# Performance work log

Measured on AMD Instinct MI355X. Metric: run time of the kernel, lower is better.

The kernel has to match this reference:

```python
import jax, jax.numpy as jnp
import numpy as np

PD = 256            # pretrain_dim == dim_in (standard mode)
DZ = 128            # dim_z
PD2 = PD + 2        # feature dim after concatenating 2-d coords
FD = PD + 2 * PD2   # final_dim = 772
TEMP = float(DZ) ** 0.5
EPS = 1e-12
N1, N2 = 4096, 2048


def _lin_init(key, din, dout):
    w = jax.random.normal(key, (dout, din), jnp.float32) * 0.02
    b = jnp.zeros((dout,), jnp.float32)
    return w, b


def _lin(x, w, b):
    return x @ w.T + b


def setup_inputs() -> dict:
    key = jax.random.key(0)
    ks = jax.random.split(key, 13)
    lm_X = jax.random.normal(ks[0], (N1, PD), jnp.float32)
    lm_Y = jax.random.normal(ks[1], (N1, 2), jnp.float32)
    tg_X = jax.random.normal(ks[2], (N2, PD), jnp.float32)
    tg_Y = jax.random.normal(ks[3], (N2, 2), jnp.float32)
    lm_delay = jax.random.uniform(ks[4], (N1,), jnp.float32)
    tg_delay = jax.random.uniform(ks[5], (N2,), jnp.float32)
    aq_w, aq_b = _lin_init(ks[6], PD, DZ)    # att_attribute q proj
    ak_w, ak_b = _lin_init(ks[7], PD, DZ)    # att_attribute k proj
    w1_w, w1_b = _lin_init(ks[8], PD2, PD2)  # self.w_1
    w2_w, w2_b = _lin_init(ks[9], PD2, PD2)  # self.w_2
    pq_w, pq_b = _lin_init(ks[10], FD, DZ)   # pred attention q proj
    pk_w, pk_b = _lin_init(ks[11], PD, DZ)   # pred attention k proj
    pv_w, pv_b = _lin_init(ks[12], 2, 2)     # pred attention v proj
    gamma1 = jnp.ones((1, 1), jnp.float32)
    gamma2 = jnp.ones((1, 1), jnp.float32)
    gamma3 = jnp.ones((1, 1), jnp.float32)
    alpha = jnp.ones((1, 1), jnp.float32)
    beta = jnp.zeros((1, 1), jnp.float32)
    return dict(lm_X=lm_X, lm_Y=lm_Y, tg_X=tg_X, tg_Y=tg_Y,
                lm_delay=lm_delay, tg_delay=tg_delay,
                aq_w=aq_w, aq_b=aq_b, ak_w=ak_w, ak_b=ak_b,
                w1_w=w1_w, w1_b=w1_b, w2_w=w2_w, w2_b=w2_b,
                pq_w=pq_w, pq_b=pq_b, pk_w=pk_w, pk_b=pk_b,
                pv_w=pv_w, pv_b=pv_b,
                gamma1=gamma1, gamma2=gamma2, gamma3=gamma3,
                alpha=alpha, beta=beta)


def reference(lm_X, lm_Y, tg_X, tg_Y, lm_delay, tg_delay,
              aq_w, aq_b, ak_w, ak_b,
              w1_w, w1_b, w2_w, w2_b,
              pq_w, pq_b, pk_w, pk_b, pv_w, pv_b,
              gamma1, gamma2, gamma3, alpha, beta):
    n2 = tg_X.shape[0]
    a = alpha[0, 0]
    b0 = beta[0, 0]

    lm_feature = jnp.concatenate([lm_X, lm_Y], axis=1)            # [N1, PD2]
    tg_feature_0 = jnp.concatenate([tg_X, jnp.zeros((n2, 2), lm_X.dtype)], axis=1)
    router_0 = jnp.mean(lm_feature, axis=0)                        # [PD2]

    delay_score = jnp.exp(-gamma1[0, 0] * (a * lm_delay + b0))     # [N1]
    rou0 = jnp.exp(-gamma2[0, 0] * (a * tg_delay + b0))            # [N2]
    rou1 = jnp.exp(-gamma3[0, 0] * (a * tg_delay + b0))            # [N2]

    # SimpleAttention1: attribute score of targets over landmarks
    q = _lin(tg_X, aq_w, aq_b)
    k = _lin(lm_X, ak_w, ak_b)
    attr = jnp.exp(jax.nn.softmax((q / TEMP) @ k.T, axis=-1))      # [N2, N1]

    # Degree-normalized propagation of adj_matrix_0 (block-structured:
    # lm rows = identity, tg rows = [attr | I | rou0-col], router row = [delay | 0 | 1]).
    deg_tg0 = 1.0 + attr.sum(axis=1) + rou0                        # [N2]
    tg_prop0 = (attr @ lm_feature + tg_feature_0 + rou0[:, None] * router_0[None, :]) \
               / (deg_tg0 + EPS)[:, None]
    router_prop0 = (delay_score @ lm_feature + router_0) / (1.0 + delay_score.sum() + EPS)

    tg_feature_1 = _lin(tg_prop0, w1_w, w1_b)                      # [N2, PD2]
    router_1 = _lin(router_prop0[None, :], w1_w, w1_b)             # [1, PD2]

    # Second propagation: adj_matrix_1 = I + rou1 on tg->router column.
    tg_prop1 = (tg_feature_1 + rou1[:, None] * router_1) / (1.0 + rou1 + EPS)[:, None]
    tg_feature_2 = _lin(tg_prop1, w2_w, w2_b)                      # [N2, PD2]

    final_tg_feature = jnp.concatenate([tg_X, tg_feature_1, tg_feature_2], axis=-1)  # [N2, FD]

    # SimpleAttention2 (collaborative MLP prediction)
    q2 = _lin(final_tg_feature, pq_w, pq_b)
    k2 = _lin(lm_X, pk_w, pk_b)
    v2 = _lin(lm_Y, pv_w, pv_b)
    attn2 = jax.nn.softmax((q2 / TEMP) @ k2.T, axis=-1)            # [N2, N1]
    y_pred = attn2 @ v2                                            # [N2, 2]
    return y_pred, final_tg_feature
```

## Files before the change

### kernel.cpp

```cpp
#include <hip/hip_runtime.h>

#define N1 4096
#define N2 2048
#define PD 256
#define DZ 128
#define PD2 258
#define PD2P 264
#define FD 772
#define FDP 776
#define APN 272
#define APLD 72
#define SPLITS 16

typedef short s8v __attribute__((ext_vector_type(8)));
typedef float f32x4 __attribute__((ext_vector_type(4)));

__device__ __forceinline__ short f2b(float f) {
    union { float f; unsigned u; } v; v.f = f;
    unsigned r = v.u + 0x7fffu + ((v.u >> 16) & 1u);
    return (short)(r >> 16);
}
__device__ __forceinline__ float sb2f(short s) {
    union { unsigned u; float f; } v;
    v.u = ((unsigned)(unsigned short)s) << 16;
    return v.f;
}

constexpr int S0 = N1 * PD;
constexpr int S1 = S0 + N2 * PD;
constexpr int S2 = S1 + DZ * PD;
constexpr int S3 = S2 + 256 * 256;
constexpr int S4 = S3 + DZ * FDP;
constexpr int S5 = S4 + PD2 * PD2P;
constexpr int S6 = S5 + PD2 * PD2P;
constexpr int S7 = S6 + APN * N1;
constexpr int S8 = S7 + N1;
constexpr int S9 = S8 + 2048 + 8192 + 12288 + 256;

__global__ __launch_bounds__(256) void cvt_all(
    const float* __restrict__ lmX, const float* __restrict__ lmY,
    const float* __restrict__ tgX,
    const float* __restrict__ aqw, const float* __restrict__ akw,
    const float* __restrict__ pkw, const float* __restrict__ pqw,
    const float* __restrict__ w1w, const float* __restrict__ w2w,
    const float* __restrict__ lmd, const float* __restrict__ tgd,
    const float* __restrict__ g1, const float* __restrict__ g2,
    const float* __restrict__ g3, const float* __restrict__ al,
    const float* __restrict__ be,
    const float* __restrict__ pvw, const float* __restrict__ pvb,
    const float* __restrict__ akb, const float* __restrict__ pkb,
    short* __restrict__ lmXb, short* __restrict__ tgXb,
    short* __restrict__ aqwb, short* __restrict__ wkkb,
    short* __restrict__ pqwb,
    short* __restrict__ w1wb, short* __restrict__ w2wb,
    short* __restrict__ lmFTb,
    float* __restrict__ dscore, float* __restrict__ rou0,
    float* __restrict__ rou1, float* __restrict__ v2b,
    float* __restrict__ Z, short* __restrict__ finalFb,
    short* __restrict__ tgp1b, float* __restrict__ biasKK,
    float* __restrict__ outF)
{
    int i = blockIdx.x * 256 + threadIdx.x;
    if (i < S0) { lmXb[i] = f2b(lmX[i]); return; }
    if (i < S1) { int j = i - S0; int r = j >> 8, c = j & 255;
                  float v = tgX[j];
                  tgXb[j] = f2b(v);
                  outF[(size_t)r * FD + c] = v;
                  finalFb[(size_t)r * FDP + c] = f2b(v); return; }
    if (i < S2) { int j = i - S1; aqwb[j] = f2b(aqw[j]); return; }
    if (i < S3) { int j = i - S2; int r = j >> 8, c = j & 255;
                  wkkb[j] = f2b(r < 128 ? akw[r * 256 + c] : pkw[(r - 128) * 256 + c]);
                  return; }
    if (i < S4) { int j = i - S3; int r = j / FDP, c = j - r * FDP;
                  pqwb[j] = (c < FD) ? f2b(pqw[r * FD + c]) : (short)0; return; }
    if (i < S5) { int j = i - S4; int r = j / PD2P, c = j - r * PD2P;
                  w1wb[j] = (c < PD2) ? f2b(w1w[r * PD2 + c]) : (short)0; return; }
    if (i < S6) { int j = i - S5; int r = j / PD2P, c = j - r * PD2P;
                  w2wb[j] = (c < PD2) ? f2b(w2w[r * PD2 + c]) : (short)0; return; }
    if (i < S7) { int j = i - S6; int c = j >> 12, r = j & (N1 - 1);
                  float v = 0.f;
                  if (c < PD) v = lmX[r * PD + c];
                  else if (c < PD2) v = lmY[r * 2 + (c - PD)];
                  else if (c == PD2) v = 1.0f;
                  lmFTb[j] = f2b(v); return; }
    if (i < S8) { int j = i - S7;
                  float a = al[0], b = be[0];
                  dscore[j] = __expf(-g1[0] * (a * lmd[j] + b));
                  float y0 = lmY[2 * j], y1 = lmY[2 * j + 1];
                  v2b[2 * j]     = pvw[0] * y0 + pvw[1] * y1 + pvb[0];
                  v2b[2 * j + 1] = pvw[2] * y0 + pvw[3] * y1 + pvb[1];
                  if (j < N2) { float t = a * tgd[j] + b;
                                rou0[j] = __expf(-g2[0] * t);
                                rou1[j] = __expf(-g3[0] * t); }
                  return; }
    if (i < S9) { int j = i - S8;
                  if (j < 2048) { Z[j] = 0.f; return; }
                  j -= 2048;
                  if (j < 8192) { int r = j >> 2, c = FD + (j & 3);
                                  finalFb[(size_t)r * FDP + c] = 0; return; }
                  j -= 8192;
                  if (j < 12288) { int r = j / 6, c = PD2 + (j - r * 6);
                                   tgp1b[(size_t)r * PD2P + c] = 0; return; }
                  j -= 12288;
                  biasKK[j] = (j < 128) ? akb[j] : pkb[j - 128];
                  return; }
}

__global__ __launch_bounds__(256) void router_kernel(const short* __restrict__ lmFTb,
                                                     const float* __restrict__ dscore,
                                                     float* __restrict__ router0,
                                                     float* __restrict__ routerp0) {
    int c = blockIdx.x;
    const short* rowp = lmFTb + (size_t)c * N1;
    __shared__ float r1[256], r2[256], r3[256];
    int tid = threadIdx.x;
    float s1 = 0.f, s2 = 0.f, s3 = 0.f;
    for (int i = tid; i < N1; i += 256) {
        float v = sb2f(rowp[i]);
        float d = dscore[i];
        s1 += v; s2 += d * v; s3 += d;
    }
    r1[tid] = s1; r2[tid] = s2; r3[tid] = s3; __syncthreads();
    for (int o = 128; o > 0; o >>= 1) {
        if (tid < o) { r1[tid] += r1[tid + o]; r2[tid] += r2[tid + o]; r3[tid] += r3[tid + o]; }
        __syncthreads();
    }
    if (tid == 0) {
        float r0 = r1[0] / (float)N1;
        router0[c] = r0;
        routerp0[c] = (r2[0] + r0) / (1.f + r3[0] + 1e-12f);
    }
}

__global__ __launch_bounds__(256) void router1_kernel(const float* __restrict__ rp0,
                                                      const float* __restrict__ w1w,
                                                      const float* __restrict__ w1b,
                                                      float* __restrict__ router1) {
    for (int c = threadIdx.x; c < PD2; c += 256) {
        float s = w1b[c];
        const float* wr = w1w + (size_t)c * PD2;
        for (int k = 0; k < PD2; ++k) s += rp0[k] * wr[k];
        router1[c] = s;
    }
}

__global__ __launch_bounds__(256) void proj_gemm(
    const short* __restrict__ A, const short* __restrict__ B,
    const float* __restrict__ bias, short* __restrict__ outB,
    int M, int N, int KP, int ldo, float scale)
{
    __shared__ short Als[64][40];
    __shared__ short Bls[64][40];
    const int tid = threadIdx.x;
    const int wave = tid >> 6, lane = tid & 63;
    const int wm = wave >> 1, wn = wave & 1;
    const int lm = lane & 15, lq = lane >> 4;
    const int row0 = blockIdx.y * 64, col0 = blockIdx.x * 64;
    f32x4 acc[2][2];
    const f32x4 zero4 = {0.f, 0.f, 0.f, 0.f};
#pragma unroll
    for (int mt = 0; mt < 2; ++mt)
#pragma unroll
        for (int nt = 0; nt < 2; ++nt) acc[mt][nt] = zero4;
    const s8v zero8 = {0, 0, 0, 0, 0, 0, 0, 0};
    for (int k0 = 0; k0 < KP; k0 += 32) {
        {
            int r = tid >> 2, cg = tid & 3;
            int gk = k0 + cg * 8;
            s8v va = zero8, vb = zero8;
            if (row0 + r < M && gk < KP) va = *(const s8v*)(A + (size_t)(row0 + r) * KP + gk);
            if (col0 + r < N && gk < KP) vb = *(const s8v*)(B + (size_t)(col0 + r) * KP + gk);
            *(s8v*)(&Als[r][cg * 8]) = va;
            *(s8v*)(&Bls[r][cg * 8]) = vb;
        }
        __syncthreads();
        s8v af[2], bf[2];
#pragma unroll
        for (int mt = 0; mt < 2; ++mt)
            af[mt] = *(const s8v*)(&Als[wm * 32 + mt * 16 + lm][lq * 8]);
#pragma unroll
        for (int nt = 0; nt < 2; ++nt)
            bf[nt] = *(const s8v*)(&Bls[wn * 32 + nt * 16 + lm][lq * 8]);
#pragma unroll
        for (int mt = 0; mt < 2; ++mt)
#pragma unroll
            for (int nt = 0; nt < 2; ++nt)
                acc[mt][nt] = __builtin_amdgcn_mfma_f32_16x16x32_bf16(
                    af[mt], bf[nt], acc[mt][nt], 0, 0, 0);
        __syncthreads();
    }
#pragma unroll
    for (int mt = 0; mt < 2; ++mt)
#pragma unroll
        for (int nt = 0; nt < 2; ++nt) {
            int c = col0 + wn * 32 + nt * 16 + lm;
            if (c >= N) continue;
            float bv = bias ? bias[c] : 0.f;
#pragma unroll
            for (int i = 0; i < 4; ++i) {
                int r = row0 + wm * 32 + mt * 16 + lq * 4 + i;
                if (r >= M) continue;
                outB[(size_t)r * ldo + c] = f2b(scale * (acc[mt][nt][i] + bv));
            }
        }
}

__global__ __launch_bounds__(256) void scores_e(
    const short* __restrict__ Q,
    const short* __restrict__ Kk,
    short* __restrict__ E, float* __restrict__ Z)
{
    __shared__ short Als[128][40];
    __shared__ short Bls[128][40];
    const int tid = threadIdx.x;
    const int wave = tid >> 6, lane = tid & 63;
    const int wm = wave >> 1, wn = wave & 1;
    const int lm = lane & 15, lq = lane >> 4;
    const int row0 = blockIdx.y * 128, col0 = blockIdx.x * 128;
    f32x4 acc[4][4];
    const f32x4 zero4 = {0.f, 0.f, 0.f, 0.f};
#pragma unroll
    for (int mt = 0; mt < 4; ++mt)
#pragma unroll
        for (int nt = 0; nt < 4; ++nt) acc[mt][nt] = zero4;
    for (int k0 = 0; k0 < 128; k0 += 32) {
#pragma unroll
        for (int l = 0; l < 2; ++l) {
            int id = l * 256 + tid;
            int r = id >> 2, cg = id & 3;
            int gk = k0 + cg * 8;
            *(s8v*)(&Als[r][cg * 8]) = *(const s8v*)(Q + (size_t)(row0 + r) * DZ + gk);
            *(s8v*)(&Bls[r][cg * 8]) = *(const s8v*)(Kk + (size_t)(col0 + r) * 256 + gk);
        }
        __syncthreads();
        s8v af[4], bf[4];
#pragma unroll
        for (int mt = 0; mt < 4; ++mt)
            af[mt] = *(const s8v*)(&Als[wm * 64 + mt * 16 + lm][lq * 8]);
#pragma unroll
        for (int nt = 0; nt < 4; ++nt)
            bf[nt] = *(const s8v*)(&Bls[wn * 64 + nt * 16 + lm][lq * 8]);
#pragma unroll
        for (int mt = 0; mt < 4; ++mt)
#pragma unroll
            for (int nt = 0; nt < 4; ++nt)
                acc[mt][nt] = __builtin_amdgcn_mfma_f32_16x16x32_bf16(
                    af[mt], bf[nt], acc[mt][nt], 0, 0, 0);
        __syncthreads();
    }
#pragma unroll
    for (int mt = 0; mt < 4; ++mt)
#pragma unroll
        for (int i = 0; i < 4; ++i) {
            int r = row0 + wm * 64 + mt * 16 + lq * 4 + i;
            float rs = 0.f;
#pragma unroll
            for (int nt = 0; nt < 4; ++nt) {
                int c = col0 + wn * 64 + nt * 16 + lm;
                float e = __expf(acc[mt][nt][i]);
                E[(size_t)r * N1 + c] = f2b(e);
                rs += e;
            }
#pragma unroll
            for (int msk = 1; msk < 16; msk <<= 1) rs += __shfl_xor(rs, msk, 64);
            if (lm == 0) atomicAdd(&Z[r], rs);
        }
}

__global__ __launch_bounds__(256) void ap_gemm(const short* __restrict__ E,
                                               const float* __restrict__ Z,
                                               const short* __restrict__ lmFTb,
                                               float* __restrict__ part)
{
    __shared__ short Als[128 * APLD];
    __shared__ short Bls[APN * APLD];
    const int tid = threadIdx.x;
    const int wave = tid >> 6, lane = tid & 63;
    const int lm = lane & 15, lq = lane >> 4;
    const int s = blockIdx.x;
    const int row0 = blockIdx.y * 128;
    const int kbase = s * (N1 / SPLITS);
    f32x4 acc0[17], acc1[17];
    const f32x4 zero4 = {0.f, 0.f, 0.f, 0.f};
#pragma unroll
    for (int nt = 0; nt < 17; ++nt) { acc0[nt] = zero4; acc1[nt] = zero4; }

    for (int it = 0; it < (N1 / SPLITS) / 64; ++it) {
        int k0 = kbase + it * 64;
#pragma unroll
        for (int l = 0; l < 4; ++l) {
            int id = l * 256 + tid;
            int r = id >> 3, g = id & 7;
            s8v ev = *(const s8v*)(E + (size_t)(row0 + r) * N1 + k0 + g * 8);
            float invZ = __builtin_amdgcn_rcpf(Z[row0 + r]);
            s8v av;
#pragma unroll
            for (int j = 0; j < 8; ++j)
                av[j] = f2b(__expf(sb2f(ev[j]) * invZ));
            *(s8v*)(&Als[r * APLD + g * 8]) = av;
        }
#pragma unroll
        for (int l = 0; l < 9; ++l) {
            int id = l * 256 + tid;
            if (id < APN * 8) {
                int r = id >> 3, g = id & 7;
                *(s8v*)(&Bls[r * APLD + g * 8]) =
                    *(const s8v*)(lmFTb + (size_t)r * N1 + k0 + g * 8);
            }
        }
        __syncthreads();
        s8v a00 = *(const s8v*)(&Als[(wave * 32 + lm) * APLD + lq * 8]);
        s8v a01 = *(const s8v*)(&Als[(wave * 32 + lm) * APLD + 32 + lq * 8]);
        s8v a10 = *(const s8v*)(&Als[(wave * 32 + 16 + lm) * APLD + lq * 8]);
        s8v a11 = *(const s8v*)(&Als[(wave * 32 + 16 + lm) * APLD + 32 + lq * 8]);
#pragma unroll
        for (int nt = 0; nt < 17; ++nt) {
            s8v b0 = *(const s8v*)(&Bls[(nt * 16 + lm) * APLD + lq * 8]);
            s8v b1 = *(const s8v*)(&Bls[(nt * 16 + lm) * APLD + 32 + lq * 8]);
            acc0[nt] = __builtin_amdgcn_mfma_f32_16x16x32_bf16(a00, b0, acc0[nt], 0, 0, 0);
            acc0[nt] = __builtin_amdgcn_mfma_f32_16x16x32_bf16(a01, b1, acc0[nt], 0, 0, 0);
            acc1[nt] = __builtin_amdgcn_mfma_f32_16x16x32_bf16(a10, b0, acc1[nt], 0, 0, 0);
            acc1[nt] = __builtin_amdgcn_mfma_f32_16x16x32_bf16(a11, b1, acc1[nt], 0, 0, 0);
        }
        __syncthreads();
    }
    float* op = part + (size_t)s * N2 * APN;
#pragma unroll
    for (int nt = 0; nt < 17; ++nt) {
        int c = nt * 16 + lm;
#pragma unroll
        for (int i = 0; i < 4; ++i) {
            int r = row0 + wave * 32 + lq * 4 + i;
            op[(size_t)r * APN + c] = acc0[nt][i];
            op[(size_t)(r + 16) * APN + c] = acc1[nt][i];
        }
    }
}

__global__ __launch_bounds__(256) void fix_tgp0(const float* __restrict__ part,
                                                const float* __restrict__ tgX,
                                                const float* __restrict__ rou0,
                                                const float* __restrict__ router0,
                                                short* __restrict__ outb) {
    int r = blockIdx.x;
    int tid = threadIdx.x;
    __shared__ float sAsum;
    float s0 = 0.f, s1 = 0.f;
#pragma unroll
    for (int s = 0; s < SPLITS; ++s)
        s0 += part[((size_t)s * N2 + r) * APN + tid];
    if (tid < 8) {
#pragma unroll
        for (int s = 0; s < SPLITS; ++s)
            s1 += part[((size_t)s * N2 + r) * APN + 256 + tid];
    }
    if (tid == 2) sAsum = s1;
    __syncthreads();
    float ro = rou0[r];
    float inv = 1.f / (1.f + sAsum + ro + 1e-12f);
    {
        float v = (s0 + tgX[(size_t)r * PD + tid] + ro * router0[tid]) * inv;
        outb[(size_t)r * PD2P + tid] = f2b(v);
    }
    if (tid < 8) {
        int c = 256 + tid;
        float v = 0.f;
        if (c < PD2) v = (s1 + ro * router0[c]) * inv;
        outb[(size_t)r * PD2P + c] = f2b(v);
    }
}

__global__ __launch_bounds__(256) void w_gemm(
    const short* __restrict__ A, const short* __restrict__ B,
    const float* __restrict__ bias,
    float* __restrict__ outFcol, short* __restrict__ fFbcol,
    const float* __restrict__ rou1, const float* __restrict__ router1,
    short* __restrict__ tgp1b)
{
    __shared__ short Als[64][40];
    __shared__ short Bls[64][40];
    const int tid = threadIdx.x;
    const int wave = tid >> 6, lane = tid & 63;
    const int wm = wave >> 1, wn = wave & 1;
    const int lm = lane & 15, lq = lane >> 4;
    const int row0 = blockIdx.y * 64, col0 = blockIdx.x * 64;
    f32x4 acc[2][2];
    const f32x4 zero4 = {0.f, 0.f, 0.f, 0.f};
#pragma unroll
    for (int mt = 0; mt < 2; ++mt)
#pragma unroll
        for (int nt = 0; nt < 2; ++nt) acc[mt][nt] = zero4;
    const s8v zero8 = {0, 0, 0, 0, 0, 0, 0, 0};
    for (int k0 = 0; k0 < PD2P; k0 += 32) {
        {
            int r = tid >> 2, cg = tid & 3;
            int gk = k0 + cg * 8;
            s8v va = zero8, vb = zero8;
            if (gk < PD2P) {
                va = *(const s8v*)(A + (size_t)(row0 + r) * PD2P + gk);
                if (col0 + r < PD2) vb = *(const s8v*)(B + (size_t)(col0 + r) * PD2P + gk);
            }
            *(s8v*)(&Als[r][cg * 8]) = va;
            *(s8v*)(&Bls[r][cg * 8]) = vb;
        }
        __syncthreads();
        s8v af[2], bf[2];
#pragma unroll
        for (int mt = 0; mt < 2; ++mt)
            af[mt] = *(const s8v*)(&Als[wm * 32 + mt * 16 + lm][lq * 8]);
#pragma unroll
        for (int nt = 0; nt < 2; ++nt)
            bf[nt] = *(const s8v*)(&Bls[wn * 32 + nt * 16 + lm][lq * 8]);
#pragma unroll
        for (int mt = 0; mt < 2; ++mt)
#pragma unroll
            for (int nt = 0; nt < 2; ++nt)
                acc[mt][nt] = __builtin_amdgcn_mfma_f32_16x16x32_bf16(
                    af[mt], bf[nt], acc[mt][nt], 0, 0, 0);
        __syncthreads();
    }
#pragma unroll
    for (int mt = 0; mt < 2; ++mt)
#pragma unroll
        for (int nt = 0; nt < 2; ++nt) {
            int c = col0 + wn * 32 + nt * 16 + lm;
            if (c >= PD2) continue;
            float bv = bias[c];
            float rc = router1 ? router1[c] : 0.f;
#pragma unroll
            for (int i = 0; i < 4; ++i) {
                int r = row0 + wm * 32 + mt * 16 + lq * 4 + i;
                float v = acc[mt][nt][i] + bv;
                outFcol[(size_t)r * FD + c] = v;
                fFbcol[(size_t)r * FDP + c] = f2b(v);
                if (tgp1b) {
                    float ro = rou1[r];
                    float t = (v + ro * rc) / (1.f + ro + 1e-12f);
                    tgp1b[(size_t)r * PD2P + c] = f2b(t);
                }
            }
        }
}

__global__ __launch_bounds__(256) void attn2_flash(
    const short* __restrict__ Q,
    const short* __restrict__ Kk,
    const float* __restrict__ V, float* __restrict__ part2)
{
    __shared__ short Qls[64 * 136];
    __shared__ short Kls[64 * 136];
    __shared__ float Vls[128];
    const int tid = threadIdx.x;
    const int wave = tid >> 6, lane = tid & 63;
    const int lm = lane & 15, lq = lane >> 4;
    const int chunk = blockIdx.x;
    const int row0 = blockIdx.y * 64;
#pragma unroll
    for (int l = 0; l < 4; ++l) {
        int id = l * 256 + tid;
        int r = id >> 4, g = id & 15;
        *(s8v*)(&Qls[r * 136 + g * 8]) = *(const s8v*)(Q + (size_t)(row0 + r) * DZ + g * 8);
    }
    __syncthreads();
    s8v af[4];
#pragma unroll
    for (int ks = 0; ks < 4; ++ks)
        af[ks] = *(const s8v*)(&Qls[(wave * 16 + lm) * 136 + ks * 32 + lq * 8]);
    float z[4] = {0.f, 0.f, 0.f, 0.f}, y0[4] = {0.f, 0.f, 0.f, 0.f}, y1[4] = {0.f, 0.f, 0.f, 0.f};

    for (int t = 0; t < 8; ++t) {
        int col0 = chunk * 512 + t * 64;
        __syncthreads();
#pragma unroll
        for (int l = 0; l < 4; ++l) {
            int id = l * 256 + tid;
            int r = id >> 4, g = id & 15;
            *(s8v*)(&Kls[r * 136 + g * 8]) =
                *(const s8v*)(Kk + (size_t)(col0 + r) * 256 + 128 + g * 8);
        }
        if (tid < 128) Vls[tid] = V[col0 * 2 + tid];
        __syncthreads();
        f32x4 acc[4];
        const f32x4 zero4 = {0.f, 0.f, 0.f, 0.f};
#pragma unroll
        for (int nt = 0; nt < 4; ++nt) acc[nt] = zero4;
#pragma unroll
        for (int nt = 0; nt < 4; ++nt)
#pragma unroll
            for (int ks = 0; ks < 4; ++ks) {
                s8v bf = *(const s8v*)(&Kls[(nt * 16 + lm) * 136 + ks * 32 + lq * 8]);
                acc[nt] = __builtin_amdgcn_mfma_f32_16x16x32_bf16(af[ks], bf, acc[nt], 0, 0, 0);
            }
        float v0[4], v1[4];
#pragma unroll
        for (int nt = 0; nt < 4; ++nt) {
            v0[nt] = Vls[(nt * 16 + lm) * 2];
            v1[nt] = Vls[(nt * 16 + lm) * 2 + 1];
        }
#pragma unroll
        for (int i = 0; i < 4; ++i) {
            float e0 = __expf(acc[0][i]), e1 = __expf(acc[1][i]);
            float e2 = __expf(acc[2][i]), e3 = __expf(acc[3][i]);
            float pz = e0 + e1 + e2 + e3;
            float py0 = e0 * v0[0] + e1 * v0[1] + e2 * v0[2] + e3 * v0[3];
            float py1 = e0 * v1[0] + e1 * v1[1] + e2 * v1[2] + e3 * v1[3];
#pragma unroll
            for (int msk = 1; msk < 16; msk <<= 1) {
                pz  += __shfl_xor(pz, msk, 64);
                py0 += __shfl_xor(py0, msk, 64);
                py1 += __shfl_xor(py1, msk, 64);
            }
            z[i] += pz; y0[i] += py0; y1[i] += py1;
        }
    }
    if (lm == 0) {
#pragma unroll
        for (int i = 0; i < 4; ++i) {
            int r = row0 + wave * 16 + lq * 4 + i;
            float* p = part2 + ((size_t)r * 8 + chunk) * 4;
            p[0] = z[i]; p[1] = y0[i]; p[2] = y1[i];
        }
    }
}

__global__ void attn2_combine(const float* __restrict__ part2, float* __restrict__ out) {
    int r = blockIdx.x * blockDim.x + threadIdx.x;
    if (r >= N2) return;
    const float* p = part2 + (size_t)r * 32;
    float Zt = 0.f, Y0 = 0.f, Y1 = 0.f;
#pragma unroll
    for (int c = 0; c < 8; ++c) {
        Zt += p[c * 4]; Y0 += p[c * 4 + 1]; Y1 += p[c * 4 + 2];
    }
    out[2 * r] = Y0 / Zt;
    out[2 * r + 1] = Y1 / Zt;
}

extern "C" void kernel_launch(void* const* d_in, const int* in_sizes, int n_in,
                              void* d_out, int out_size, void* d_ws, size_t ws_size,
                              hipStream_t stream) {
    const float* lm_X = (const float*)d_in[0];
    const float* lm_Y = (const float*)d_in[1];
    const float* tg_X = (const float*)d_in[2];
    const float* lm_delay = (const float*)d_in[4];
    const float* tg_delay = (const float*)d_in[5];
    const float* aq_w = (const float*)d_in[6];
    const float* aq_b = (const float*)d_in[7];
    const float* ak_w = (const float*)d_in[8];
    const float* ak_b = (const float*)d_in[9];
    const float* w1_w = (const float*)d_in[10];
    const float* w1_b = (const float*)d_in[11];
    const float* w2_w = (const float*)d_in[12];
    const float* w2_b = (const float*)d_in[13];
    const float* pq_w = (const float*)d_in[14];
    const float* pq_b = (const float*)d_in[15];
    const float* pk_w = (const float*)d_in[16];
    const float* pk_b = (const float*)d_in[17];
    const float* pv_w = (const float*)d_in[18];
    const float* pv_b = (const float*)d_in[19];
    const float* g1 = (const float*)d_in[20];
    const float* g2 = (const float*)d_in[21];
    const float* g3 = (const float*)d_in[22];
    const float* al = (const float*)d_in[23];
    const float* be = (const float*)d_in[24];

    float* out = (float*)d_out;
    float* outF = out + (size_t)N2 * 2;

    char* base = (char*)d_ws;
    size_t off = 0;
    auto allocF = [&](size_t n) -> float* {
        float* p = (float*)(base + off);
        off += (n * 4 + 255) / 256 * 256;
        return p;
    };
    auto allocS = [&](size_t n) -> short* {
        short* p = (short*)(base + off);
        off += (n * 2 + 255) / 256 * 256;
        return p;
    };

    short* E        = allocS((size_t)N2 * N1);
    float* appart   = allocF((size_t)SPLITS * N2 * APN);
    short* lmFTb    = allocS((size_t)APN * N1);
    short* lmXb     = allocS((size_t)N1 * PD);
    short* tgXb     = allocS((size_t)N2 * PD);
    short* qb_b     = allocS((size_t)N2 * DZ);
    short* kk       = allocS((size_t)N1 * 256);
    short* q2_b     = allocS((size_t)N2 * DZ);
    short* tgp0b    = allocS((size_t)N2 * PD2P);
    short* tgp1b    = allocS((size_t)N2 * PD2P);
    short* finalFb  = allocS((size_t)N2 * FDP);
    short* aqwb     = allocS((size_t)DZ * PD);
    short* wkkb     = allocS((size_t)256 * 256);
    short* pqwb     = allocS((size_t)DZ * FDP);
    short* w1wb     = allocS((size_t)PD2 * PD2P);
    short* w2wb     = allocS((size_t)PD2 * PD2P);
    float* v2b      = allocF((size_t)N1 * 2);
    float* part2    = allocF((size_t)N2 * 32);
    float* Zbuf     = allocF(N2);
    float* biasKK   = allocF(256);
    float* router0  = allocF(PD2);
    float* routerp0 = allocF(PD2);
    float* router1  = allocF(PD2);
    float* dscore   = allocF(N1);
    float* rou0     = allocF(N2);
    float* rou1     = allocF(N2);

    const float INV_TEMP = 0.08838834764831845f;

    hipLaunchKernelGGL(cvt_all, dim3((S9 + 255) / 256), dim3(256), 0, stream,
                       lm_X, lm_Y, tg_X, aq_w, ak_w, pk_w, pq_w, w1_w, w2_w,
                       lm_delay, tg_delay, g1, g2, g3, al, be, pv_w, pv_b, ak_b, pk_b,
                       lmXb, tgXb, aqwb, wkkb, pqwb, w1wb, w2wb, lmFTb,
                       dscore, rou0, rou1, v2b, Zbuf, finalFb, tgp1b, biasKK, outF);
    hipLaunchKernelGGL(router_kernel, dim3(PD2), dim3(256), 0, stream,
                       lmFTb, dscore, router0, routerp0);
    hipLaunchKernelGGL(router1_kernel, dim3(1), dim3(256), 0, stream,
                       routerp0, w1_w, w1_b, router1);

    hipLaunchKernelGGL(proj_gemm, dim3(4, 64), dim3(256), 0, stream,
                       lmXb, wkkb, biasKK, kk, N1, 256, PD, 256, 1.f);
    hipLaunchKernelGGL(proj_gemm, dim3(2, 32), dim3(256), 0, stream,
                       tgXb, aqwb, aq_b, qb_b, N2, DZ, PD, DZ, INV_TEMP);
    hipLaunchKernelGGL(scores_e, dim3(32, 16), dim3(256), 0, stream, qb_b, kk, E, Zbuf);
    hipLaunchKernelGGL(ap_gemm, dim3(SPLITS, N2 / 128), dim3(256), 0, stream,
                       E, Zbuf, lmFTb, appart);
    hipLaunchKernelGGL(fix_tgp0, dim3(N2), dim3(256), 0, stream,
                       appart, tg_X, rou0, router0, tgp0b);
    hipLaunchKernelGGL(w_gemm, dim3(5, 32), dim3(256), 0, stream,
                       tgp0b, w1wb, w1_b, outF + 256, finalFb + 256, rou1, router1, tgp1b);
    hipLaunchKernelGGL(w_gemm, dim3(5, 32), dim3(256), 0, stream,
                       tgp1b, w2wb, w2_b, outF + 514, finalFb + 514,
                       nullptr, nullptr, nullptr);
    hipLaunchKernelGGL(proj_gemm, dim3(2, 32), dim3(256), 0, stream,
                       finalFb, pqwb, pq_b, q2_b, N2, DZ, FDP, DZ, INV_TEMP);
    hipLaunchKernelGGL(attn2_flash, dim3(8, N2 / 64), dim3(256), 0, stream,
                       q2_b, kk, v2b, part2);
    hipLaunchKernelGGL(attn2_combine, dim3((N2 + 255) / 256), dim3(256), 0, stream,
                       part2, out);
}
```

Measured before the change: 252.2 us.

## Fuse router, projection and combine kernels; convert weights inline; bf16 partials

Merges the router reductions with the K/Q projection GEMMs into one kernel that converts fp32 inputs to bf16 while staging into LDS. This drops the separate bf16 copies of lmX, tgX and the projection weights. It also folds router1 into the scores kernel as an extra block, makes the ap_gemm partials bf16 with a new 512-thread launch, and replaces attn2_combine with a last-block-done atomic reduction. The goal is fewer launches and less intermediate memory traffic, at the cost of precision in the partials and an extra memset.

```diff
diff --git a/kernel.cpp b/kernel.cpp
--- a/kernel.cpp
+++ b/kernel.cpp
@@ -26,64 +26,51 @@
     return v.f;
 }
 
-constexpr int S0 = N1 * PD;
-constexpr int S1 = S0 + N2 * PD;
-constexpr int S2 = S1 + DZ * PD;
-constexpr int S3 = S2 + 256 * 256;
-constexpr int S4 = S3 + DZ * FDP;
-constexpr int S5 = S4 + PD2 * PD2P;
-constexpr int S6 = S5 + PD2 * PD2P;
-constexpr int S7 = S6 + APN * N1;
-constexpr int S8 = S7 + N1;
-constexpr int S9 = S8 + 2048 + 8192 + 12288 + 256;
+constexpr int R0 = N2 * PD;
+constexpr int R1 = R0 + PD2 * PD2P;
+constexpr int R2 = R1 + PD2 * PD2P;
+constexpr int R3 = R2 + DZ * FDP;
+constexpr int R4 = R3 + APN * N1;
+constexpr int R5 = R4 + 4096;
+constexpr int R6 = R5 + 2048;
+constexpr int R7 = R6 + N2 * 4;
+constexpr int R8 = R7 + N2 * 6;
 
 __global__ __launch_bounds__(256) void cvt_all(
     const float* __restrict__ lmX, const float* __restrict__ lmY,
     const float* __restrict__ tgX,
-    const float* __restrict__ aqw, const float* __restrict__ akw,
-    const float* __restrict__ pkw, const float* __restrict__ pqw,
-    const float* __restrict__ w1w, const float* __restrict__ w2w,
+    const float* __restrict__ pqw, const float* __restrict__ w1w,
+    const float* __restrict__ w2w,
     const float* __restrict__ lmd, const float* __restrict__ tgd,
     const float* __restrict__ g1, const float* __restrict__ g2,
     const float* __restrict__ g3, const float* __restrict__ al,
     const float* __restrict__ be,
     const float* __restrict__ pvw, const float* __restrict__ pvb,
-    const float* __restrict__ akb, const float* __restrict__ pkb,
-    short* __restrict__ lmXb, short* __restrict__ tgXb,
-    short* __restrict__ aqwb, short* __restrict__ wkkb,
-    short* __restrict__ pqwb,
     short* __restrict__ w1wb, short* __restrict__ w2wb,
-    short* __restrict__ lmFTb,
+    short* __restrict__ pqwb, short* __restrict__ lmFTb,
     float* __restrict__ dscore, float* __restrict__ rou0,
     float* __restrict__ rou1, float* __restrict__ v2b,
     float* __restrict__ Z, short* __restrict__ finalFb,
-    short* __restrict__ tgp1b, float* __restrict__ biasKK,
-    float* __restrict__ outF)
+    short* __restrict__ tgp1b, float* __restrict__ outF)
 {
     int i = blockIdx.x * 256 + threadIdx.x;
-    if (i < S0) { lmXb[i] = f2b(lmX[i]); return; }
-    if (i < S1) { int j = i - S0; int r = j >> 8, c = j & 255;
-                  float v = tgX[j];
-                  tgXb[j] = f2b(v);
+    if (i < R0) { int r = i >> 8, c = i & 255;
+                  float v = tgX[i];
                   outF[(size_t)r * FD + c] = v;
                   finalFb[(size_t)r * FDP + c] = f2b(v); return; }
-    if (i < S2) { int j = i - S1; aqwb[j] = f2b(aqw[j]); return; }
-    if (i < S3) { int j = i - S2; int r = j >> 8, c = j & 255;
-                  wkkb[j] = f2b(r < 128 ? akw[r * 256 + c] : pkw[(r - 128) * 256 + c]);
-                  return; }
-    if (i < S4) { int j = i - S3; int r = j / FDP, c = j - r * FDP;
+    if (i < R1) { int j = i - R0; int r = j / PD2P, c = j - r * PD2P;
+                  w1wb[j] = (c < PD2) ? f2b(w1w[r * PD2 + c]) : (short)0; return; }
+    if (i < R2) { int j = i - R1; int r = j / PD2P, c = j - r * PD2P;
+                  w2wb[j] = (c < PD2) ? f2b(w2w[r * PD2 + c]) : (short)0; return; }
+    if (i < R3) { int j = i - R2; int r = j / FDP, c = j - r * FDP;
                   pqwb[j] = (c < FD) ? f2b(pqw[r * FD + c]) : (short)0; return; }
-    if (i < S5) { int j = i - S4; int r = j / PD2P, c = j - r * PD2P;
-                  w1wb[j] = (c < PD2) ? f2b(w1w[r * PD2 + c]) : (short)0; return; }
-    if (i < S6) { int j = i - S5; int r = j / PD2P, c = j - r * PD2P;
-                  w2wb[j] = (c < PD2) ? f2b(w2w[r * PD2 + c]) : (short)0; return; }
-    if (i < S7) { int j = i - S6; int c = j >> 12, r = j & (N1 - 1);
+    if (i < R4) { int j = i - R3; int c = j >> 12, r = j & (N1 - 1);
                   float v = 0.f;
-                  if (c < PD) v = lmX[r * PD + c];
+                  if (c < PD) v = lmX[(size_t)r * PD + c];
                   else if (c < PD2) v = lmY[r * 2 + (c - PD)];
                   else if (c == PD2) v = 1.0f;
                   lmFTb[j] = f2b(v); return; }
-    if (i < S8) { int j = i - S7;
+    if (i < R5) { int j = i - R4;
                   float a = al[0], b = be[0];
                   dscore[j] = __expf(-g1[0] * (a * lmd[j] + b));
                   float y0 = lmY[2 * j], y1 = lmY[2 * j + 1];
@@ -93,132 +80,167 @@
                                 rou0[j] = __expf(-g2[0] * t);
                                 rou1[j] = __expf(-g3[0] * t); }
                   return; }
-    if (i < S9) { int j = i - S8;
-                  if (j < 2048) { Z[j] = 0.f; return; }
-                  j -= 2048;
-                  if (j < 8192) { int r = j >> 2, c = FD + (j & 3);
-                                  finalFb[(size_t)r * FDP + c] = 0; return; }
-                  j -= 8192;
-                  if (j < 12288) { int r = j / 6, c = PD2 + (j - r * 6);
-                                   tgp1b[(size_t)r * PD2P + c] = 0; return; }
-                  j -= 12288;
-                  biasKK[j] = (j < 128) ? akb[j] : pkb[j - 128];
-                  return; }
-}
-
-__global__ __launch_bounds__(256) void router_kernel(const short* __restrict__ lmFTb,
-                                                     const float* __restrict__ dscore,
-                                                     float* __restrict__ router0,
-                                                     float* __restrict__ routerp0) {
-    int c = blockIdx.x;
-    const short* rowp = lmFTb + (size_t)c * N1;
-    __shared__ float r1[256], r2[256], r3[256];
-    int tid = threadIdx.x;
-    float s1 = 0.f, s2 = 0.f, s3 = 0.f;
-    for (int i = tid; i < N1; i += 256) {
-        float v = sb2f(rowp[i]);
-        float d = dscore[i];
-        s1 += v; s2 += d * v; s3 += d;
-    }
-    r1[tid] = s1; r2[tid] = s2; r3[tid] = s3; __syncthreads();
-    for (int o = 128; o > 0; o >>= 1) {
-        if (tid < o) { r1[tid] += r1[tid + o]; r2[tid] += r2[tid + o]; r3[tid] += r3[tid + o]; }
-        __syncthreads();
-    }
-    if (tid == 0) {
-        float r0 = r1[0] / (float)N1;
-        router0[c] = r0;
-        routerp0[c] = (r2[0] + r0) / (1.f + r3[0] + 1e-12f);
-    }
-}
-
-__global__ __launch_bounds__(256) void router1_kernel(const float* __restrict__ rp0,
-                                                      const float* __restrict__ w1w,
-                                                      const float* __restrict__ w1b,
-                                                      float* __restrict__ router1) {
-    for (int c = threadIdx.x; c < PD2; c += 256) {
-        float s = w1b[c];
-        const float* wr = w1w + (size_t)c * PD2;
-        for (int k = 0; k < PD2; ++k) s += rp0[k] * wr[k];
-        router1[c] = s;
-    }
-}
-
-__global__ __launch_bounds__(256) void proj_gemm(
-    const short* __restrict__ A, const short* __restrict__ B,
-    const float* __restrict__ bias, short* __restrict__ outB,
-    int M, int N, int KP, int ldo, float scale)
+    if (i < R6) { Z[i - R5] = 0.f; return; }
+    if (i < R7) { int j = i - R6; int r = j >> 2;
+                  finalFb[(size_t)r * FDP + FD + (j & 3)] = 0; return; }
+    if (i < R8) { int j = i - R7; int r = j / 6;
+                  tgp1b[(size_t)r * PD2P + PD2 + (j - r * 6)] = 0; return; }
+}
+
+__global__ __launch_bounds__(256) void rkq_kernel(
+    const float* __restrict__ lmX, const float* __restrict__ tgX,
+    const float* __restrict__ aqw, const float* __restrict__ aqb,
+    const float* __restrict__ akw, const float* __restrict__ akb,
+    const float* __restrict__ pkw, const float* __restrict__ pkb,
+    const short* __restrict__ lmFTb, const float* __restrict__ dscore,
+    float* __restrict__ router0, float* __restrict__ routerp0,
+    short* __restrict__ kk, short* __restrict__ qb)
 {
-    __shared__ short Als[64][40];
-    __shared__ short Bls[64][40];
-    const int tid = threadIdx.x;
-    const int wave = tid >> 6, lane = tid & 63;
-    const int wm = wave >> 1, wn = wave & 1;
+    __shared__ __align__(16) short LDS[5120];
+    const int j = blockIdx.x, tid = threadIdx.x;
+    const int lane = tid & 63, wv = tid >> 6;
+    const int wm = wv >> 1, wn = wv & 1;
     const int lm = lane & 15, lq = lane >> 4;
-    const int row0 = blockIdx.y * 64, col0 = blockIdx.x * 64;
-    f32x4 acc[2][2];
     const f32x4 zero4 = {0.f, 0.f, 0.f, 0.f};
-#pragma unroll
-    for (int mt = 0; mt < 2; ++mt)
-#pragma unroll
-        for (int nt = 0; nt < 2; ++nt) acc[mt][nt] = zero4;
-    const s8v zero8 = {0, 0, 0, 0, 0, 0, 0, 0};
-    for (int k0 = 0; k0 < KP; k0 += 32) {
-        {
-            int r = tid >> 2, cg = tid & 3;
-            int gk = k0 + cg * 8;
-            s8v va = zero8, vb = zero8;
-            if (row0 + r < M && gk < KP) va = *(const s8v*)(A + (size_t)(row0 + r) * KP + gk);
-            if (col0 + r < N && gk < KP) vb = *(const s8v*)(B + (size_t)(col0 + r) * KP + gk);
-            *(s8v*)(&Als[r][cg * 8]) = va;
-            *(s8v*)(&Bls[r][cg * 8]) = vb;
-        }
-        __syncthreads();
-        s8v af[2], bf[2];
+
+    if (j < 258) {
+        float* r1 = (float*)LDS;
+        float* r2 = r1 + 256;
+        float* r3 = r2 + 256;
+        const short* rowp = lmFTb + (size_t)j * N1;
+        float s1 = 0.f, s2 = 0.f, s3 = 0.f;
+        for (int i = tid; i < N1; i += 256) {
+            float v = sb2f(rowp[i]);
+            float d = dscore[i];
+            s1 += v; s2 += d * v; s3 += d;
+        }
+        r1[tid] = s1; r2[tid] = s2; r3[tid] = s3; __syncthreads();
+        for (int o = 128; o > 0; o >>= 1) {
+            if (tid < o) { r1[tid] += r1[tid + o]; r2[tid] += r2[tid + o]; r3[tid] += r3[tid + o]; }
+            __syncthreads();
+        }
+        if (tid == 0) {
+            float r0v = r1[0] / (float)N1;
+            router0[j] = r0v;
+            routerp0[j] = (r2[0] + r0v) / (1.f + r3[0] + 1e-12f);
+        }
+        return;
+    }
+    short* Als = LDS;
+    short* Bls = LDS + 64 * 40;
+    f32x4 acc[2][2] = {{zero4, zero4}, {zero4, zero4}};
+    const int r = tid >> 2, cgp = tid & 3;
+    if (j < 514) {
+        int jt = j - 258;
+        int row0 = (jt >> 2) * 64, col0 = (jt & 3) * 64;
+        for (int k0 = 0; k0 < 256; k0 += 32) {
+            int gk = k0 + cgp * 8;
+            const float* ap = lmX + (size_t)(row0 + r) * PD + gk;
+            int c = col0 + r;
+            const float* bp = (c < 128) ? akw + (size_t)c * PD + gk
+                                        : pkw + (size_t)(c - 128) * PD + gk;
+            s8v va, vb;
+#pragma unroll
+            for (int q = 0; q < 8; ++q) { va[q] = f2b(ap[q]); vb[q] = f2b(bp[q]); }
+            *(s8v*)(Als + r * 40 + cgp * 8) = va;
+            *(s8v*)(Bls + r * 40 + cgp * 8) = vb;
+            __syncthreads();
+            s8v af[2], bf[2];
+#pragma unroll
+            for (int mt = 0; mt < 2; ++mt)
+                af[mt] = *(const s8v*)(Als + (wm * 32 + mt * 16 + lm) * 40 + lq * 8);
+#pragma unroll
+            for (int nt = 0; nt < 2; ++nt)
+                bf[nt] = *(const s8v*)(Bls + (wn * 32 + nt * 16 + lm) * 40 + lq * 8);
+#pragma unroll
+            for (int mt = 0; mt < 2; ++mt)
+#pragma unroll
+                for (int nt = 0; nt < 2; ++nt)
+                    acc[mt][nt] = __builtin_amdgcn_mfma_f32_16x16x32_bf16(
+                        af[mt], bf[nt], acc[mt][nt], 0, 0, 0);
+            __syncthreads();
+        }
 #pragma unroll
         for (int mt = 0; mt < 2; ++mt)
-            af[mt] = *(const s8v*)(&Als[wm * 32 + mt * 16 + lm][lq * 8]);
-#pragma unroll
-        for (int nt = 0; nt < 2; ++nt)
-            bf[nt] = *(const s8v*)(&Bls[wn * 32 + nt * 16 + lm][lq * 8]);
+#pragma unroll
+            for (int nt = 0; nt < 2; ++nt) {
+                int c = col0 + wn * 32 + nt * 16 + lm;
+                float bv = (c < 128) ? akb[c] : pkb[c - 128];
+#pragma unroll
+                for (int i = 0; i < 4; ++i) {
+                    int rr = row0 + wm * 32 + mt * 16 + lq * 4 + i;
+                    kk[(size_t)rr * 256 + c] = f2b(acc[mt][nt][i] + bv);
+                }
+            }
+    } else {
+        int jt = j - 514;
+        int row0 = (jt >> 1) * 64, col0 = (jt & 1) * 64;
+        for (int k0 = 0; k0 < 256; k0 += 32) {
+            int gk = k0 + cgp * 8;
+            const float* ap = tgX + (size_t)(row0 + r) * PD + gk;
+            const float* bp = aqw + (size_t)(col0 + r) * PD + gk;
+            s8v va, vb;
+#pragma unroll
+            for (int q = 0; q < 8; ++q) { va[q] = f2b(ap[q]); vb[q] = f2b(bp[q]); }
+            *(s8v*)(Als + r * 40 + cgp * 8) = va;
+            *(s8v*)(Bls + r * 40 + cgp * 8) = vb;
+            __syncthreads();
+            s8v af[2], bf[2];
+#pragma unroll
+            for (int mt = 0; mt < 2; ++mt)
+                af[mt] = *(const s8v*)(Als + (wm * 32 + mt * 16 + lm) * 40 + lq * 8);
+#pragma unroll
+            for (int nt = 0; nt < 2; ++nt)
+                bf[nt] = *(const s8v*)(Bls + (wn * 32 + nt * 16 + lm) * 40 + lq * 8);
+#pragma unroll
+            for (int mt = 0; mt < 2; ++mt)
+#pragma unroll
+                for (int nt = 0; nt < 2; ++nt)
+                    acc[mt][nt] = __builtin_amdgcn_mfma_f32_16x16x32_bf16(
+                        af[mt], bf[nt], acc[mt][nt], 0, 0, 0);
+            __syncthreads();
+        }
+        const float INV_TEMP = 0.08838834764831845f;
 #pragma unroll
         for (int mt = 0; mt < 2; ++mt)
 #pragma unroll
-            for (int nt = 0; nt < 2; ++nt)
-                acc[mt][nt] = __builtin_amdgcn_mfma_f32_16x16x32_bf16(
-                    af[mt], bf[nt], acc[mt][nt], 0, 0, 0);
-        __syncthreads();
-    }
-#pragma unroll
-    for (int mt = 0; mt < 2; ++mt)
-#pragma unroll
-        for (int nt = 0; nt < 2; ++nt) {
-            int c = col0 + wn * 32 + nt * 16 + lm;
-            if (c >= N) continue;
-            float bv = bias ? bias[c] : 0.f;
-#pragma unroll
-            for (int i = 0; i < 4; ++i) {
-                int r = row0 + wm * 32 + mt * 16 + lq * 4 + i;
-                if (r >= M) continue;
-                outB[(size_t)r * ldo + c] = f2b(scale * (acc[mt][nt][i] + bv));
-            }
-        }
+            for (int nt = 0; nt < 2; ++nt) {
+                int c = col0 + wn * 32 + nt * 16 + lm;
+                float bv = aqb[c];
+#pragma unroll
+                for (int i = 0; i < 4; ++i) {
+                    int rr = row0 + wm * 32 + mt * 16 + lq * 4 + i;
+                    qb[(size_t)rr * DZ + c] = f2b(INV_TEMP * (acc[mt][nt][i] + bv));
+                }
+            }
+    }
 }
 
 __global__ __launch_bounds__(256) void scores_e(
-    const short* __restrict__ Q,
-    const short* __restrict__ Kk,
-    short* __restrict__ E, float* __restrict__ Z)
+    const short* __restrict__ Q, const short* __restrict__ Kk,
+    short* __restrict__ E, float* __restrict__ Z,
+    const float* __restrict__ rp0, const float* __restrict__ w1w,
+    const float* __restrict__ w1b, float* __restrict__ router1)
 {
-    __shared__ short Als[128][40];
-    __shared__ short Bls[128][40];
-    const int tid = threadIdx.x;
-    const int wave = tid >> 6, lane = tid & 63;
-    const int wm = wave >> 1, wn = wave & 1;
+    const int j = blockIdx.x, tid = threadIdx.x;
+    if (j == 512) {
+        for (int c = tid; c < PD2; c += 256) {
+            float s = w1b[c];
+            const float* wr = w1w + (size_t)c * PD2;
+            for (int k = 0; k < PD2; ++k) s += rp0[k] * wr[k];
+            router1[c] = s;
+        }
+        return;
+    }
+    __shared__ __align__(16) short LDS[10240];
+    short* Als = LDS;
+    short* Bls = LDS + 128 * 40;
+    const int lane = tid & 63, wv = tid >> 6;
+    const int wm = wv >> 1, wn = wv & 1;
     const int lm = lane & 15, lq = lane >> 4;
-    const int row0 = blockIdx.y * 128, col0 = blockIdx.x * 128;
+    const int row0 = (j >> 5) * 128, col0 = (j & 31) * 128;
+    const f32x4 zero4 = {0.f, 0.f, 0.f, 0.f};
     f32x4 acc[4][4];
-    const f32x4 zero4 = {0.f, 0.f, 0.f, 0.f};
 #pragma unroll
     for (int mt = 0; mt < 4; ++mt)
 #pragma unroll
@@ -227,19 +249,19 @@
 #pragma unroll
         for (int l = 0; l < 2; ++l) {
             int id = l * 256 + tid;
-            int r = id >> 2, cg = id & 3;
-            int gk = k0 + cg * 8;
-            *(s8v*)(&Als[r][cg * 8]) = *(const s8v*)(Q + (size_t)(row0 + r) * DZ + gk);
-            *(s8v*)(&Bls[r][cg * 8]) = *(const s8v*)(Kk + (size_t)(col0 + r) * 256 + gk);
+            int r = id >> 2, cgp = id & 3;
+            int gk = k0 + cgp * 8;
+            *(s8v*)(Als + r * 40 + cgp * 8) = *(const s8v*)(Q + (size_t)(row0 + r) * DZ + gk);
+            *(s8v*)(Bls + r * 40 + cgp * 8) = *(const s8v*)(Kk + (size_t)(col0 + r) * 256 + gk);
         }
         __syncthreads();
         s8v af[4], bf[4];
 #pragma unroll
         for (int mt = 0; mt < 4; ++mt)
-            af[mt] = *(const s8v*)(&Als[wm * 64 + mt * 16 + lm][lq * 8]);
+            af[mt] = *(const s8v*)(Als + (wm * 64 + mt * 16 + lm) * 40 + lq * 8);
 #pragma unroll
         for (int nt = 0; nt < 4; ++nt)
-            bf[nt] = *(const s8v*)(&Bls[wn * 64 + nt * 16 + lm][lq * 8]);
+            bf[nt] = *(const s8v*)(Bls + (wn * 64 + nt * 16 + lm) * 40 + lq * 8);
 #pragma unroll
         for (int mt = 0; mt < 4; ++mt)
 #pragma unroll
@@ -267,77 +289,71 @@
         }
 }
 
-__global__ __launch_bounds__(256) void ap_gemm(const short* __restrict__ E,
+__global__ __launch_bounds__(512) void ap_gemm(const short* __restrict__ E,
                                                const float* __restrict__ Z,
                                                const short* __restrict__ lmFTb,
-                                               float* __restrict__ part)
+                                               short* __restrict__ part)
 {
-    __shared__ short Als[128 * APLD];
-    __shared__ short Bls[APN * APLD];
-    const int tid = threadIdx.x;
-    const int wave = tid >> 6, lane = tid & 63;
+    __shared__ __align__(16) short LDS[28800];
+    const int tid = threadIdx.x, bid = blockIdx.x;
+    const int lane = tid & 63, w8 = tid >> 6;
     const int lm = lane & 15, lq = lane >> 4;
-    const int s = blockIdx.x;
-    const int row0 = blockIdx.y * 128;
+    const int s = bid & 15, row0 = (bid >> 4) * 128;
     const int kbase = s * (N1 / SPLITS);
-    f32x4 acc0[17], acc1[17];
+    short* Als = LDS;
+    short* Bls = LDS + 128 * APLD;
     const f32x4 zero4 = {0.f, 0.f, 0.f, 0.f};
-#pragma unroll
-    for (int nt = 0; nt < 17; ++nt) { acc0[nt] = zero4; acc1[nt] = zero4; }
-
+    f32x4 acc[17];
+#pragma unroll
+    for (int nt = 0; nt < 17; ++nt) acc[nt] = zero4;
     for (int it = 0; it < (N1 / SPLITS) / 64; ++it) {
         int k0 = kbase + it * 64;
 #pragma unroll
-        for (int l = 0; l < 4; ++l) {
-            int id = l * 256 + tid;
-            int r = id >> 3, g = id & 7;
-            s8v ev = *(const s8v*)(E + (size_t)(row0 + r) * N1 + k0 + g * 8);
+        for (int l = 0; l < 2; ++l) {
+            int id = l * 512 + tid;
+            int r = id >> 3, gg = id & 7;
+            s8v ev = *(const s8v*)(E + (size_t)(row0 + r) * N1 + k0 + gg * 8);
             float invZ = __builtin_amdgcn_rcpf(Z[row0 + r]);
             s8v av;
 #pragma unroll
-            for (int j = 0; j < 8; ++j)
-                av[j] = f2b(__expf(sb2f(ev[j]) * invZ));
-            *(s8v*)(&Als[r * APLD + g * 8]) = av;
-        }
-#pragma unroll
-        for (int l = 0; l < 9; ++l) {
-            int id = l * 256 + tid;
+            for (int q = 0; q < 8; ++q)
+                av[q] = f2b(__expf(sb2f(ev[q]) * invZ));
+            *(s8v*)(Als + r * APLD + gg * 8) = av;
+        }
+#pragma unroll
+        for (int l = 0; l < 5; ++l) {
+            int id = l * 512 + tid;
             if (id < APN * 8) {
-                int r = id >> 3, g = id & 7;
-                *(s8v*)(&Bls[r * APLD + g * 8]) =
-                    *(const s8v*)(lmFTb + (size_t)r * N1 + k0 + g * 8);
-            }
-        }
-        __syncthreads();
-        s8v a00 = *(const s8v*)(&Als[(wave * 32 + lm) * APLD + lq * 8]);
-        s8v a01 = *(const s8v*)(&Als[(wave * 32 + lm) * APLD + 32 + lq * 8]);
-        s8v a10 = *(const s8v*)(&Als[(wave * 32 + 16 + lm) * APLD + lq * 8]);
-        s8v a11 = *(const s8v*)(&Als[(wave * 32 + 16 + lm) * APLD + 32 + lq * 8]);
+                int r = id >> 3, gg = id & 7;
+                *(s8v*)(Bls + r * APLD + gg * 8) =
+                    *(const s8v*)(lmFTb + (size_t)r * N1 + k0 + gg * 8);
+            }
+        }
+        __syncthreads();
+        s8v a0 = *(const s8v*)(Als + (w8 * 16 + lm) * APLD + lq * 8);
+        s8v a1 = *(const s8v*)(Als + (w8 * 16 + lm) * APLD + 32 + lq * 8);
 #pragma unroll
         for (int nt = 0; nt < 17; ++nt) {
-            s8v b0 = *(const s8v*)(&Bls[(nt * 16 + lm) * APLD + lq * 8]);
-            s8v b1 = *(const s8v*)(&Bls[(nt * 16 + lm) * APLD + 32 + lq * 8]);
-            acc0[nt] = __builtin_amdgcn_mfma_f32_16x16x32_bf16(a00, b0, acc0[nt], 0, 0, 0);
-            acc0[nt] = __builtin_amdgcn_mfma_f32_16x16x32_bf16(a01, b1, acc0[nt], 0, 0, 0);
-            acc1[nt] = __builtin_amdgcn_mfma_f32_16x16x32_bf16(a10, b0, acc1[nt], 0, 0, 0);
-            acc1[nt] = __builtin_amdgcn_mfma_f32_16x16x32_bf16(a11, b1, acc1[nt], 0, 0, 0);
-        }
-        __syncthreads();
-    }
-    float* op = part + (size_t)s * N2 * APN;
+            s8v b0 = *(const s8v*)(Bls + (nt * 16 + lm) * APLD + lq * 8);
+            s8v b1 = *(const s8v*)(Bls + (nt * 16 + lm) * APLD + 32 + lq * 8);
+            acc[nt] = __builtin_amdgcn_mfma_f32_16x16x32_bf16(a0, b0, acc[nt], 0, 0, 0);
+            acc[nt] = __builtin_amdgcn_mfma_f32_16x16x32_bf16(a1, b1, acc[nt], 0, 0, 0);
+        }
+        __syncthreads();
+    }
+    short* op = part + (size_t)s * N2 * APN;
 #pragma unroll
     for (int nt = 0; nt < 17; ++nt) {
         int c = nt * 16 + lm;
 #pragma unroll
         for (int i = 0; i < 4; ++i) {
-            int r = row0 + wave * 32 + lq * 4 + i;
-            op[(size_t)r * APN + c] = acc0[nt][i];
-            op[(size_t)(r + 16) * APN + c] = acc1[nt][i];
-        }
-    }
-}
-
-__global__ __launch_bounds__(256) void fix_tgp0(const float* __restrict__ part,
+            int r = row0 + w8 * 16 + lq * 4 + i;
+            op[(size_t)r * APN + c] = f2b(acc[nt][i]);
+        }
+    }
+}
+
+__global__ __launch_bounds__(256) void fix_tgp0(const short* __restrict__ part,
                                                 const float* __restrict__ tgX,
                                                 const float* __restrict__ rou0,
                                                 const float* __restrict__ router0,
@@ -348,11 +364,11 @@
     float s0 = 0.f, s1 = 0.f;
 #pragma unroll
     for (int s = 0; s < SPLITS; ++s)
-        s0 += part[((size_t)s * N2 + r) * APN + tid];
+        s0 += sb2f(part[((size_t)s * N2 + r) * APN + tid]);
     if (tid < 8) {
 #pragma unroll
         for (int s = 0; s < SPLITS; ++s)
-            s1 += part[((size_t)s * N2 + r) * APN + 256 + tid];
+            s1 += sb2f(part[((size_t)s * N2 + r) * APN + 256 + tid]);
     }
     if (tid == 2) sAsum = s1;
     __syncthreads();
@@ -377,40 +393,35 @@
     const float* __restrict__ rou1, const float* __restrict__ router1,
     short* __restrict__ tgp1b)
 {
-    __shared__ short Als[64][40];
-    __shared__ short Bls[64][40];
+    __shared__ __align__(16) short LDS[5120];
+    short* Als = LDS;
+    short* Bls = LDS + 64 * 40;
     const int tid = threadIdx.x;
-    const int wave = tid >> 6, lane = tid & 63;
-    const int wm = wave >> 1, wn = wave & 1;
+    const int lane = tid & 63, wv = tid >> 6;
+    const int wm = wv >> 1, wn = wv & 1;
     const int lm = lane & 15, lq = lane >> 4;
     const int row0 = blockIdx.y * 64, col0 = blockIdx.x * 64;
-    f32x4 acc[2][2];
     const f32x4 zero4 = {0.f, 0.f, 0.f, 0.f};
-#pragma unroll
-    for (int mt = 0; mt < 2; ++mt)
-#pragma unroll
-        for (int nt = 0; nt < 2; ++nt) acc[mt][nt] = zero4;
+    f32x4 acc[2][2] = {{zero4, zero4}, {zero4, zero4}};
     const s8v zero8 = {0, 0, 0, 0, 0, 0, 0, 0};
+    const int r = tid >> 2, cgp = tid & 3;
     for (int k0 = 0; k0 < PD2P; k0 += 32) {
-        {
-            int r = tid >> 2, cg = tid & 3;
-            int gk = k0 + cg * 8;
-            s8v va = zero8, vb = zero8;
-            if (gk < PD2P) {
-                va = *(const s8v*)(A + (size_t)(row0 + r) * PD2P + gk);
-                if (col0 + r < PD2) vb = *(const s8v*)(B + (size_t)(col0 + r) * PD2P + gk);
-            }
-            *(s8v*)(&Als[r][cg * 8]) = va;
-            *(s8v*)(&Bls[r][cg * 8]) = vb;
-        }
+        int gk = k0 + cgp * 8;
+        s8v va = zero8, vb = zero8;
+        if (gk < PD2P) {
+            va = *(const s8v*)(A + (size_t)(row0 + r) * PD2P + gk);
+            if (col0 + r < PD2) vb = *(const s8v*)(B + (size_t)(col0 + r) * PD2P + gk);
+        }
+        *(s8v*)(Als + r * 40 + cgp * 8) = va;
+        *(s8v*)(Bls + r * 40 + cgp * 8) = vb;
         __syncthreads();
         s8v af[2], bf[2];
 #pragma unroll
         for (int mt = 0; mt < 2; ++mt)
-            af[mt] = *(const s8v*)(&Als[wm * 32 + mt * 16 + lm][lq * 8]);
+            af[mt] = *(const s8v*)(Als + (wm * 32 + mt * 16 + lm) * 40 + lq * 8);
 #pragma unroll
         for (int nt = 0; nt < 2; ++nt)
-            bf[nt] = *(const s8v*)(&Bls[wn * 32 + nt * 16 + lm][lq * 8]);
+            bf[nt] = *(const s8v*)(Bls + (wn * 32 + nt * 16 + lm) * 40 + lq * 8);
 #pragma unroll
         for (int mt = 0; mt < 2; ++mt)
 #pragma unroll
@@ -429,45 +440,103 @@
             float rc = router1 ? router1[c] : 0.f;
 #pragma unroll
             for (int i = 0; i < 4; ++i) {
-                int r = row0 + wm * 32 + mt * 16 + lq * 4 + i;
+                int rr = row0 + wm * 32 + mt * 16 + lq * 4 + i;
                 float v = acc[mt][nt][i] + bv;
-                outFcol[(size_t)r * FD + c] = v;
-                fFbcol[(size_t)r * FDP + c] = f2b(v);
+                outFcol[(size_t)rr * FD + c] = v;
+                fFbcol[(size_t)rr * FDP + c] = f2b(v);
                 if (tgp1b) {
-                    float ro = rou1[r];
-                    float t = (v + ro * rc) / (1.f + ro + 1e-12f);
-                    tgp1b[(size_t)r * PD2P + c] = f2b(t);
+                    float ro = rou1[rr];
+                    tgp1b[(size_t)rr * PD2P + c] =
+                        f2b((v + ro * rc) / (1.f + ro + 1e-12f));
                 }
             }
         }
 }
 
+__global__ __launch_bounds__(256) void q2_gemm(
+    const short* __restrict__ A, const short* __restrict__ B,
+    const float* __restrict__ bias, short* __restrict__ outB)
+{
+    __shared__ __align__(16) short LDS[5120];
+    short* Als = LDS;
+    short* Bls = LDS + 64 * 40;
+    const int tid = threadIdx.x;
+    const int lane = tid & 63, wv = tid >> 6;
+    const int wm = wv >> 1, wn = wv & 1;
+    const int lm = lane & 15, lq = lane >> 4;
+    const int row0 = blockIdx.y * 64, col0 = blockIdx.x * 64;
+    const f32x4 zero4 = {0.f, 0.f, 0.f, 0.f};
+    f32x4 acc[2][2] = {{zero4, zero4}, {zero4, zero4}};
+    const s8v zero8 = {0, 0, 0, 0, 0, 0, 0, 0};
+    const int r = tid >> 2, cgp = tid & 3;
+    for (int k0 = 0; k0 < FDP; k0 += 32) {
+        int gk = k0 + cgp * 8;
+        s8v va = zero8, vb = zero8;
+        if (gk < FDP) {
+            va = *(const s8v*)(A + (size_t)(row0 + r) * FDP + gk);
+            vb = *(const s8v*)(B + (size_t)(col0 + r) * FDP + gk);
+        }
+        *(s8v*)(Als + r * 40 + cgp * 8) = va;
+        *(s8v*)(Bls + r * 40 + cgp * 8) = vb;
+        __syncthreads();
+        s8v af[2], bf[2];
+#pragma unroll
+        for (int mt = 0; mt < 2; ++mt)
+            af[mt] = *(const s8v*)(Als + (wm * 32 + mt * 16 + lm) * 40 + lq * 8);
+#pragma unroll
+        for (int nt = 0; nt < 2; ++nt)
+            bf[nt] = *(const s8v*)(Bls + (wn * 32 + nt * 16 + lm) * 40 + lq * 8);
+#pragma unroll
+        for (int mt = 0; mt < 2; ++mt)
+#pragma unroll
+            for (int nt = 0; nt < 2; ++nt)
+                acc[mt][nt] = __builtin_amdgcn_mfma_f32_16x16x32_bf16(
+                    af[mt], bf[nt], acc[mt][nt], 0, 0, 0);
+        __syncthreads();
+    }
+    const float INV_TEMP = 0.08838834764831845f;
+#pragma unroll
+    for (int mt = 0; mt < 2; ++mt)
+#pragma unroll
+        for (int nt = 0; nt < 2; ++nt) {
+            int c = col0 + wn * 32 + nt * 16 + lm;
+            float bv = bias[c];
+#pragma unroll
+            for (int i = 0; i < 4; ++i) {
+                int rr = row0 + wm * 32 + mt * 16 + lq * 4 + i;
+                outB[(size_t)rr * DZ + c] = f2b(INV_TEMP * (acc[mt][nt][i] + bv));
+            }
+        }
+}
+
 __global__ __launch_bounds__(256) void attn2_flash(
-    const short* __restrict__ Q,
-    const short* __restrict__ Kk,
-    const float* __restrict__ V, float* __restrict__ part2)
+    const short* __restrict__ Q, const short* __restrict__ Kk,
+    const float* __restrict__ V, float* __restrict__ part2,
+    unsigned* __restrict__ done, float* __restrict__ out)
 {
-    __shared__ short Qls[64 * 136];
-    __shared__ short Kls[64 * 136];
+    __shared__ __align__(16) short Qls[64 * 136];
+    __shared__ __align__(16) short Kls[64 * 136];
     __shared__ float Vls[128];
+    __shared__ unsigned sdone;
     const int tid = threadIdx.x;
-    const int wave = tid >> 6, lane = tid & 63;
+    const int lane = tid & 63, wv = tid >> 6;
     const int lm = lane & 15, lq = lane >> 4;
-    const int chunk = blockIdx.x;
-    const int row0 = blockIdx.y * 64;
+    const int chunk = blockIdx.x & 7, row0 = (blockIdx.x >> 3) * 64;
+    const f32x4 zero4 = {0.f, 0.f, 0.f, 0.f};
 #pragma unroll
     for (int l = 0; l < 4; ++l) {
         int id = l * 256 + tid;
         int r = id >> 4, g = id & 15;
-        *(s8v*)(&Qls[r * 136 + g * 8]) = *(const s8v*)(Q + (size_t)(row0 + r) * DZ + g * 8);
+        *(s8v*)(Qls + r * 136 + g * 8) = *(const s8v*)(Q + (size_t)(row0 + r) * DZ + g * 8);
     }
     __syncthreads();
     s8v af[4];
 #pragma unroll
     for (int ks = 0; ks < 4; ++ks)
-        af[ks] = *(const s8v*)(&Qls[(wave * 16 + lm) * 136 + ks * 32 + lq * 8]);
-    float z[4] = {0.f, 0.f, 0.f, 0.f}, y0[4] = {0.f, 0.f, 0.f, 0.f}, y1[4] = {0.f, 0.f, 0.f, 0.f};
-
+        af[ks] = *(const s8v*)(Qls + (wv * 16 + lm) * 136 + ks * 32 + lq * 8);
+    float z[4] = {0.f, 0.f, 0.f, 0.f};
+    float y0[4] = {0.f, 0.f, 0.f, 0.f};
+    float y1[4] = {0.f, 0.f, 0.f, 0.f};
     for (int t = 0; t < 8; ++t) {
         int col0 = chunk * 512 + t * 64;
         __syncthreads();
@@ -475,20 +544,19 @@
         for (int l = 0; l < 4; ++l) {
             int id = l * 256 + tid;
             int r = id >> 4, g = id & 15;
-            *(s8v*)(&Kls[r * 136 + g * 8]) =
+            *(s8v*)(Kls + r * 136 + g * 8) =
                 *(const s8v*)(Kk + (size_t)(col0 + r) * 256 + 128 + g * 8);
         }
         if (tid < 128) Vls[tid] = V[col0 * 2 + tid];
         __syncthreads();
         f32x4 acc[4];
-        const f32x4 zero4 = {0.f, 0.f, 0.f, 0.f};
 #pragma unroll
         for (int nt = 0; nt < 4; ++nt) acc[nt] = zero4;
 #pragma unroll
         for (int nt = 0; nt < 4; ++nt)
 #pragma unroll
             for (int ks = 0; ks < 4; ++ks) {
-                s8v bf = *(const s8v*)(&Kls[(nt * 16 + lm) * 136 + ks * 32 + lq * 8]);
+                s8v bf = *(const s8v*)(Kls + (nt * 16 + lm) * 136 + ks * 32 + lq * 8);
                 acc[nt] = __builtin_amdgcn_mfma_f32_16x16x32_bf16(af[ks], bf, acc[nt], 0, 0, 0);
             }
         float v0[4], v1[4];
@@ -516,24 +584,28 @@
     if (lm == 0) {
 #pragma unroll
         for (int i = 0; i < 4; ++i) {
-            int r = row0 + wave * 16 + lq * 4 + i;
-            float* p = part2 + ((size_t)r * 8 + chunk) * 4;
-            p[0] = z[i]; p[1] = y0[i]; p[2] = y1[i];
-        }
-    }
-}
-
-__global__ void attn2_combine(const float* __restrict__ part2, float* __restrict__ out) {
-    int r = blockIdx.x * blockDim.x + threadIdx.x;
-    if (r >= N2) return;
-    const float* p = part2 + (size_t)r * 32;
-    float Zt = 0.f, Y0 = 0.f, Y1 = 0.f;
-#pragma unroll
-    for (int c = 0; c < 8; ++c) {
-        Zt += p[c * 4]; Y0 += p[c * 4 + 1]; Y1 += p[c * 4 + 2];
-    }
-    out[2 * r] = Y0 / Zt;
-    out[2 * r + 1] = Y1 / Zt;
+            int r = row0 + wv * 16 + lq * 4 + i;
+            float* pp = part2 + ((size_t)r * 8 + chunk) * 4;
+            pp[0] = z[i]; pp[1] = y0[i]; pp[2] = y1[i];
+        }
+    }
+    __threadfence();
+    __syncthreads();
+    if (tid == 0) sdone = atomicAdd(done, 1u);
+    __syncthreads();
+    if (sdone == 255u) {
+        __threadfence();
+        for (int r = tid; r < N2; r += 256) {
+            const float* pp = part2 + (size_t)r * 32;
+            float Zt = 0.f, Y0 = 0.f, Y1 = 0.f;
+#pragma unroll
+            for (int c = 0; c < 8; ++c) {
+                Zt += pp[c * 4]; Y0 += pp[c * 4 + 1]; Y1 += pp[c * 4 + 2];
+            }
+            out[2 * r] = Y0 / Zt;
+            out[2 * r + 1] = Y1 / Zt;
+        }
+    }
 }
 
 extern "C" void kernel_launch(void* const* d_in, const int* in_sizes, int n_in,
@@ -570,62 +642,52 @@
     char* base = (char*)d_ws;
     size_t off = 0;
     auto allocF = [&](size_t n) -> float* {
-        float* p = (float*)(base + off);
+        float* q = (float*)(base + off);
         off += (n * 4 + 255) / 256 * 256;
-        return p;
+        return q;
     };
     auto allocS = [&](size_t n) -> short* {
-        short* p = (short*)(base + off);
+        short* q = (short*)(base + off);
         off += (n * 2 + 255) / 256 * 256;
-        return p;
+        return q;
     };
 
     short* E        = allocS((size_t)N2 * N1);
-    float* appart   = allocF((size_t)SPLITS * N2 * APN);
+    short* appart   = allocS((size_t)SPLITS * N2 * APN);
     short* lmFTb    = allocS((size_t)APN * N1);
-    short* lmXb     = allocS((size_t)N1 * PD);
-    short* tgXb     = allocS((size_t)N2 * PD);
-    short* qb_b     = allocS((size_t)N2 * DZ);
+    short* qb       = allocS((size_t)N2 * DZ);
     short* kk       = allocS((size_t)N1 * 256);
-    short* q2_b     = allocS((size_t)N2 * DZ);
+    short* q2       = allocS((size_t)N2 * DZ);
     short* tgp0b    = allocS((size_t)N2 * PD2P);
     short* tgp1b    = allocS((size_t)N2 * PD2P);
     short* finalFb  = allocS((size_t)N2 * FDP);
-    short* aqwb     = allocS((size_t)DZ * PD);
-    short* wkkb     = allocS((size_t)256 * 256);
-    short* pqwb     = allocS((size_t)DZ * FDP);
     short* w1wb     = allocS((size_t)PD2 * PD2P);
     short* w2wb     = allocS((size_t)PD2 * PD2P);
+    short* pqwb     = allocS((size_t)DZ * FDP);
     float* v2b      = allocF((size_t)N1 * 2);
     float* part2    = allocF((size_t)N2 * 32);
     float* Zbuf     = allocF(N2);
-    float* biasKK   = allocF(256);
     float* router0  = allocF(PD2);
     float* routerp0 = allocF(PD2);
     float* router1  = allocF(PD2);
     float* dscore   = allocF(N1);
     float* rou0     = allocF(N2);
     float* rou1     = allocF(N2);
-
-    const float INV_TEMP = 0.08838834764831845f;
-
-    hipLaunchKernelGGL(cvt_all, dim3((S9 + 255) / 256), dim3(256), 0, stream,
-                       lm_X, lm_Y, tg_X, aq_w, ak_w, pk_w, pq_w, w1_w, w2_w,
-                       lm_delay, tg_delay, g1, g2, g3, al, be, pv_w, pv_b, ak_b, pk_b,
-                       lmXb, tgXb, aqwb, wkkb, pqwb, w1wb, w2wb, lmFTb,
-                       dscore, rou0, rou1, v2b, Zbuf, finalFb, tgp1b, biasKK, outF);
-    hipLaunchKernelGGL(router_kernel, dim3(PD2), dim3(256), 0, stream,
-                       lmFTb, dscore, router0, routerp0);
-    hipLaunchKernelGGL(router1_kernel, dim3(1), dim3(256), 0, stream,
-                       routerp0, w1_w, w1_b, router1);
-
-    hipLaunchKernelGGL(proj_gemm, dim3(4, 64), dim3(256), 0, stream,
-                       lmXb, wkkb, biasKK, kk, N1, 256, PD, 256, 1.f);
-    hipLaunchKernelGGL(proj_gemm, dim3(2, 32), dim3(256), 0, stream,
-                       tgXb, aqwb, aq_b, qb_b, N2, DZ, PD, DZ, INV_TEMP);
-    hipLaunchKernelGGL(scores_e, dim3(32, 16), dim3(256), 0, stream, qb_b, kk, E, Zbuf);
-    hipLaunchKernelGGL(ap_gemm, dim3(SPLITS, N2 / 128), dim3(256), 0, stream,
-                       E, Zbuf, lmFTb, appart);
+    unsigned* done  = (unsigned*)allocF(64);
+
+    hipMemsetAsync(done, 0, 256, stream);
+
+    hipLaunchKernelGGL(cvt_all, dim3((R8 + 255) / 256), dim3(256), 0, stream,
+                       lm_X, lm_Y, tg_X, pq_w, w1_w, w2_w,
+                       lm_delay, tg_delay, g1, g2, g3, al, be, pv_w, pv_b,
+                       w1wb, w2wb, pqwb, lmFTb,
+                       dscore, rou0, rou1, v2b, Zbuf, finalFb, tgp1b, outF);
+    hipLaunchKernelGGL(rkq_kernel, dim3(578), dim3(256), 0, stream,
+                       lm_X, tg_X, aq_w, aq_b, ak_w, ak_b, pk_w, pk_b,
+                       lmFTb, dscore, router0, routerp0, kk, qb);
+    hipLaunchKernelGGL(scores_e, dim3(513), dim3(256), 0, stream,
+                       qb, kk, E, Zbuf, routerp0, w1_w, w1_b, router1);
+    hipLaunchKernelGGL(ap_gemm, dim3(256), dim3(512), 0, stream, E, Zbuf, lmFTb, appart);
     hipLaunchKernelGGL(fix_tgp0, dim3(N2), dim3(256), 0, stream,
                        appart, tg_X, rou0, router0, tgp0b);
     hipLaunchKernelGGL(w_gemm, dim3(5, 32), dim3(256), 0, stream,
@@ -633,10 +695,8 @@
     hipLaunchKernelGGL(w_gemm, dim3(5, 32), dim3(256), 0, stream,
                        tgp1b, w2wb, w2_b, outF + 514, finalFb + 514,
                        nullptr, nullptr, nullptr);
-    hipLaunchKernelGGL(proj_gemm, dim3(2, 32), dim3(256), 0, stream,
-                       finalFb, pqwb, pq_b, q2_b, N2, DZ, FDP, DZ, INV_TEMP);
-    hipLaunchKernelGGL(attn2_flash, dim3(8, N2 / 64), dim3(256), 0, stream,
-                       q2_b, kk, v2b, part2);
-    hipLaunchKernelGGL(attn2_combine, dim3((N2 + 255) / 256), dim3(256), 0, stream,
-                       part2, out);
-}
+    hipLaunchKernelGGL(q2_gemm, dim3(2, 32), dim3(256), 0, stream,
+                       finalFb, pqwb, pq_b, q2);
+    hipLaunchKernelGGL(attn2_flash, dim3(256), dim3(256), 0, stream,
+                       q2, kk, v2b, part2, done, out);
+}
```

Measured after the change: 253.5 us. Within noise of the previous version (+0.5%).
